# Kernel tuning notes

Measured on AMD Instinct MI355X. Metric: run time of the kernel, lower is better.

Reference implementation:

```python
import jax, jax.numpy as jnp
import numpy as np

WH, WW = 7, 7
NUM_HEADS = 16
DIM = 512
NW = 64  # windows per image (56/7)^2


def _relative_position_index(wh, ww):
    coords = np.stack(np.meshgrid(np.arange(wh), np.arange(ww), indexing='ij'))  # 2,wh,ww
    cf = coords.reshape(2, -1)
    rel = cf[:, :, None] - cf[:, None, :]            # 2,N,N
    rel = rel.transpose(1, 2, 0).astype(np.int32)    # N,N,2
    rel[:, :, 0] += wh - 1
    rel[:, :, 1] += ww - 1
    rel[:, :, 0] *= 2 * ww - 1
    return jnp.asarray(rel.sum(-1))                  # N,N int32


def setup_inputs() -> dict:
    key = jax.random.key(0)
    ks = jax.random.split(key, 7)
    B_, N, C = 2048, WH * WW, DIM
    x = jax.random.normal(ks[0], (B_, N, C), dtype=jnp.float32)
    # 0 / -100 shifted-window mask pattern
    mask = jnp.where(jax.random.uniform(ks[1], (NW, N, N)) < 0.8, 0.0, -100.0).astype(jnp.float32)
    qkv_w = jax.random.normal(ks[2], (3 * C, C), dtype=jnp.float32) * 0.02
    qkv_b = jax.random.normal(ks[3], (3 * C,), dtype=jnp.float32) * 0.02
    proj_w = jax.random.normal(ks[4], (C, C), dtype=jnp.float32) * 0.02
    proj_b = jax.random.normal(ks[5], (C,), dtype=jnp.float32) * 0.02
    rel_bias_table = jax.random.normal(ks[6], ((2 * WH - 1) * (2 * WW - 1), NUM_HEADS), dtype=jnp.float32) * 0.02
    rel_index = _relative_position_index(WH, WW)
    return {"x": x, "mask": mask, "qkv_w": qkv_w, "qkv_b": qkv_b,
            "proj_w": proj_w, "proj_b": proj_b,
            "rel_bias_table": rel_bias_table, "rel_index": rel_index}


def reference(x, mask, qkv_w, qkv_b, proj_w, proj_b, rel_bias_table, rel_index):
    B_, N, C = x.shape
    H = NUM_HEADS
    hd = C // H
    scale = hd ** -0.5
    qkv = x @ qkv_w.T + qkv_b                         # B_,N,3C
    qkv = qkv.reshape(B_, N, 3, H, hd).transpose(2, 0, 3, 1, 4)  # 3,B_,H,N,hd
    q, k, v = qkv[0] * scale, qkv[1], qkv[2]
    attn = jnp.einsum('bhnd,bhmd->bhnm', q, k)        # B_,H,N,N
    # gathered relative position bias -> H,N,N
    bias = rel_bias_table[rel_index.reshape(-1)].reshape(N, N, H).transpose(2, 0, 1)
    attn = attn + bias[None]
    nW = mask.shape[0]
    attn = attn.reshape(B_ // nW, nW, H, N, N) + mask[None, :, None]
    attn = jax.nn.softmax(attn.reshape(B_, H, N, N), axis=-1)
    out = jnp.einsum('bhnm,bhmd->bhnd', attn, v).transpose(0, 2, 1, 3).reshape(B_, N, C)
    return out @ proj_w.T + proj_b
```

## Files before the change

### kernel.cpp

```cpp
#include <hip/hip_runtime.h>

typedef unsigned short u16;
typedef short s16x8 __attribute__((ext_vector_type(8)));
typedef __bf16 bf16x8 __attribute__((ext_vector_type(8)));
typedef float f32x4 __attribute__((ext_vector_type(4)));


__device__ __forceinline__ u16 f2bf(float f) {
  union { float f; unsigned u; } x; x.f = f;
  unsigned r = (x.u + 0x7fffu + ((x.u >> 16) & 1u)) >> 16;
  return (u16)r;
}

__device__ __forceinline__ f32x4 mfma_bf16_16x16x32(s16x8 a, s16x8 b, f32x4 c) {
  return __builtin_amdgcn_mfma_f32_16x16x32_bf16(
      __builtin_bit_cast(bf16x8, a), __builtin_bit_cast(bf16x8, b), c, 0, 0, 0);
}

__device__ __forceinline__ void gl_lds16(const u16* g, u16* l) {
  __builtin_amdgcn_global_load_lds(
      (__attribute__((address_space(1))) unsigned int*)g,
      (__attribute__((address_space(3))) unsigned int*)l, 16, 0, 0);
}

__device__ __forceinline__ int p_idx(int row, int col) {
  return row * 64 + ((((col >> 3) ^ (row & 7)) << 3) | (col & 7));
}


__global__ __launch_bounds__(256) void cvt_bf16(const float* __restrict__ src,
                                                u16* __restrict__ dst, int n) {
  int i = (blockIdx.x * 256 + threadIdx.x) * 4;
  if (i + 3 < n) {
    float4 f = *(const float4*)(src + i);
    ushort4 o;
    o.x = f2bf(f.x); o.y = f2bf(f.y); o.z = f2bf(f.z); o.w = f2bf(f.w);
    *(ushort4*)(dst + i) = o;
  }
}

__global__ __launch_bounds__(256) void build_bias(const float* __restrict__ tbl,
                                                  const int* __restrict__ ridx,
                                                  float* __restrict__ biasf) {
  int t = blockIdx.x * 256 + threadIdx.x;
  if (t < 16 * 2401) {
    int h = t / 2401, ij = t % 2401;
    biasf[t] = tbl[ridx[ij] * 16 + h];
  }
}


template <bool OUT_BF16>
__global__ __launch_bounds__(256) void gemm_bt(const u16* __restrict__ A,
                                               const u16* __restrict__ B,
                                               const float* __restrict__ bias,
                                               void* __restrict__ C,
                                               int M, int N, int K) {
  __shared__ u16 As[2][128 * 32];
  __shared__ u16 Bs[2][128 * 32];
  const int t = threadIdx.x;
  const int w = t >> 6, l = t & 63;
  const int quad = l >> 4, lo = l & 15;

  int bx = blockIdx.x, by = blockIdx.y;
  {
    const int nwg = gridDim.x * gridDim.y;
    if ((nwg & 7) == 0) {
      const int lin = bx + gridDim.x * by;
      const int swz = (lin & 7) * (nwg >> 3) + (lin >> 3);
      bx = swz % gridDim.x;
      by = swz / gridDim.x;
    }
  }
  const long m0 = (long)by * 128;
  const long n0 = (long)bx * 128;
  const int wm = (w >> 1) * 64, wn = (w & 1) * 64;

  f32x4 acc[4][4] = {};

  const int srow0 = w * 32 + (l >> 2);
  const int skc = ((l & 3) ^ ((srow0 >> 1) & 3)) * 8;
  const u16* gA = A + (m0 + srow0) * (long)K + skc;
  const u16* gB = B + (n0 + srow0) * (long)K + skc;
  const int lofs = (w * 128 + l) * 8;

  const int NT = K >> 5;

  gl_lds16(gA, As[0] + lofs);
  gl_lds16(gA + 16 * (long)K, As[0] + lofs + 64 * 8);
  gl_lds16(gB, Bs[0] + lofs);
  gl_lds16(gB + 16 * (long)K, Bs[0] + lofs + 64 * 8);
  __syncthreads();

  int cur = 0;
  for (int t0 = 0; t0 < NT; ++t0) {
    if (t0 + 1 < NT) {
      const int k0 = (t0 + 1) << 5;
      gl_lds16(gA + k0, As[cur ^ 1] + lofs);
      gl_lds16(gA + 16 * (long)K + k0, As[cur ^ 1] + lofs + 64 * 8);
      gl_lds16(gB + k0, Bs[cur ^ 1] + lofs);
      gl_lds16(gB + 16 * (long)K + k0, Bs[cur ^ 1] + lofs + 64 * 8);
    }

    const u16* as = As[cur];
    const u16* bs = Bs[cur];
    s16x8 af[4], bfv[4];
#pragma unroll
    for (int i = 0; i < 4; ++i) {
      const int ra = wm + i * 16 + lo;
      const int rb = wn + i * 16 + lo;
      af[i]  = *(const s16x8*)(as + ra * 32 + ((quad ^ ((ra >> 1) & 3)) << 3));
      bfv[i] = *(const s16x8*)(bs + rb * 32 + ((quad ^ ((rb >> 1) & 3)) << 3));
    }
#pragma unroll
    for (int mt = 0; mt < 4; ++mt)
#pragma unroll
      for (int nt = 0; nt < 4; ++nt)
        acc[mt][nt] = mfma_bf16_16x16x32(af[mt], bfv[nt], acc[mt][nt]);

    __syncthreads();
    cur ^= 1;
  }

#pragma unroll
  for (int mt = 0; mt < 4; ++mt) {
#pragma unroll
    for (int nt = 0; nt < 4; ++nt) {
      long col = n0 + wn + nt * 16 + lo;
      float bv = bias[col];
      long rowb = m0 + wm + mt * 16 + quad * 4;
#pragma unroll
      for (int r = 0; r < 4; ++r) {
        float v = acc[mt][nt][r] + bv;
        long off = (rowb + r) * (long)N + col;
        if (OUT_BF16) ((u16*)C)[off] = f2bf(v);
        else          ((float*)C)[off] = v;
      }
    }
  }
}


__global__ __launch_bounds__(256) void attn_kernel(const u16* __restrict__ qkv,
                                                   const float* __restrict__ biasf,
                                                   const float* __restrict__ mask,
                                                   u16* __restrict__ ao) {
  __shared__ u16 P[4][64 * 64];
  const int t = threadIdx.x;
  const int w = t >> 6, l = t & 63;
  const int quad = l >> 4, lo = l & 15;
  const int u = blockIdx.x * 4 + w;
  const int b = u >> 4, h = u & 15;

  const u16* qp = qkv + (long)b * 49 * 1536 + h * 32;
  const u16* kp = qp + 512;
  const u16* vp = qp + 1024;

  const s16x8 zero8 = {};
  s16x8 qf[4], kf[4];
#pragma unroll
  for (int mt = 0; mt < 4; ++mt) {
    int m = mt * 16 + lo;
    qf[mt] = (m < 49) ? *(const s16x8*)(qp + (long)m * 1536 + quad * 8) : zero8;
    kf[mt] = (m < 49) ? *(const s16x8*)(kp + (long)m * 1536 + quad * 8) : zero8;
  }

  f32x4 S[4][4] = {};
#pragma unroll
  for (int mt = 0; mt < 4; ++mt)
#pragma unroll
    for (int nt = 0; nt < 4; ++nt)
      S[mt][nt] = mfma_bf16_16x16x32(qf[mt], kf[nt], S[mt][nt]);

  const float scale = 0.17677669529663687f;
  const float* bh = biasf + h * 2401;
  const float* mw = mask + (long)(b & 63) * 2401;

#pragma unroll
  for (int mt = 0; mt < 4; ++mt) {
#pragma unroll
    for (int r = 0; r < 4; ++r) {
      int row = mt * 16 + quad * 4 + r;
      int rr = row < 49 ? row : 48;
      float vals[4];
#pragma unroll
      for (int nt = 0; nt < 4; ++nt) {
        int col = nt * 16 + lo;
        vals[nt] = (col < 49)
                       ? S[mt][nt][r] * scale + bh[rr * 49 + col] + mw[rr * 49 + col]
                       : -1e30f;
      }
      float rm = fmaxf(fmaxf(vals[0], vals[1]), fmaxf(vals[2], vals[3]));
#pragma unroll
      for (int off = 1; off < 16; off <<= 1) rm = fmaxf(rm, __shfl_xor(rm, off, 16));
      float s = 0.f;
#pragma unroll
      for (int nt = 0; nt < 4; ++nt) {
        vals[nt] = __expf(vals[nt] - rm);
        s += vals[nt];
      }
#pragma unroll
      for (int off = 1; off < 16; off <<= 1) s += __shfl_xor(s, off, 16);
      float is = 1.f / s;
#pragma unroll
      for (int nt = 0; nt < 4; ++nt) S[mt][nt][r] = vals[nt] * is;
    }
  }

  u16* pw = &P[w][0];
#pragma unroll
  for (int mt = 0; mt < 4; ++mt)
#pragma unroll
    for (int nt = 0; nt < 4; ++nt)
#pragma unroll
      for (int r = 0; r < 4; ++r)
        pw[p_idx(mt * 16 + quad * 4 + r, nt * 16 + lo)] = f2bf(S[mt][nt][r]);

  f32x4 O[4][2] = {};
#pragma unroll
  for (int kt = 0; kt < 2; ++kt) {
    s16x8 vb[2];
#pragma unroll
    for (int nt = 0; nt < 2; ++nt) {
      union { u16 us[8]; s16x8 v; } tb;
#pragma unroll
      for (int jj = 0; jj < 8; ++jj) {
        int j = kt * 32 + quad * 8 + jj;
        tb.us[jj] = (j < 49) ? vp[(long)j * 1536 + nt * 16 + lo] : (u16)0;
      }
      vb[nt] = tb.v;
    }
#pragma unroll
    for (int mt = 0; mt < 4; ++mt) {
      s16x8 pa = *(const s16x8*)(pw + p_idx(mt * 16 + lo, kt * 32 + quad * 8));
      O[mt][0] = mfma_bf16_16x16x32(pa, vb[0], O[mt][0]);
      O[mt][1] = mfma_bf16_16x16x32(pa, vb[1], O[mt][1]);
    }
  }

  u16* op = ao + (long)b * 49 * 512 + h * 32;
#pragma unroll
  for (int mt = 0; mt < 4; ++mt)
#pragma unroll
    for (int nt = 0; nt < 2; ++nt)
#pragma unroll
      for (int r = 0; r < 4; ++r) {
        int row = mt * 16 + quad * 4 + r;
        if (row < 49) op[(long)row * 512 + nt * 16 + lo] = f2bf(O[mt][nt][r]);
      }
}


extern "C" void kernel_launch(void* const* d_in, const int* in_sizes, int n_in,
                              void* d_out, int out_size, void* d_ws, size_t ws_size,
                              hipStream_t stream) {
  const float* x      = (const float*)d_in[0];
  const float* mask   = (const float*)d_in[1];
  const float* qkv_w  = (const float*)d_in[2];
  const float* qkv_b  = (const float*)d_in[3];
  const float* proj_w = (const float*)d_in[4];
  const float* proj_b = (const float*)d_in[5];
  const float* tbl    = (const float*)d_in[6];
  const int*   ridx   = (const int*)d_in[7];

  u16* xb    = (u16*)d_ws;
  u16* qkvb  = xb + 51380224;
  u16* wq    = qkvb + 154140672;
  u16* wp    = wq + 786432;
  float* biasf = (float*)(wp + 262144);

  cvt_bf16<<<50176, 256, 0, stream>>>(x, xb, 51380224);
  cvt_bf16<<<768, 256, 0, stream>>>(qkv_w, wq, 786432);
  cvt_bf16<<<256, 256, 0, stream>>>(proj_w, wp, 262144);
  build_bias<<<151, 256, 0, stream>>>(tbl, ridx, biasf);

  gemm_bt<true><<<dim3(12, 784), 256, 0, stream>>>(xb, wq, qkv_b, qkvb,
                                                   100352, 1536, 512);
  attn_kernel<<<8192, 256, 0, stream>>>(qkvb, biasf, mask, xb);

  gemm_bt<false><<<dim3(4, 784), 256, 0, stream>>>(xb, wp, proj_b, d_out,
                                                   100352, 512, 512);
}
```

Baseline: 899.5 us.

## Triple-buffer GEMM LDS tiles with prefetch distance two and partial vmcnt waits

```diff
diff --git a/kernel.cpp b/kernel.cpp
--- a/kernel.cpp
+++ b/kernel.cpp
@@ -56,8 +56,8 @@
                                                const float* __restrict__ bias,
                                                void* __restrict__ C,
                                                int M, int N, int K) {
-  __shared__ u16 As[2][128 * 32];
-  __shared__ u16 Bs[2][128 * 32];
+  __shared__ u16 As[3][128 * 32];
+  __shared__ u16 Bs[3][128 * 32];
   const int t = threadIdx.x;
   const int w = t >> 6, l = t & 63;
   const int quad = l >> 4, lo = l & 15;
@@ -86,21 +86,25 @@
 
   const int NT = K >> 5;
 
-  gl_lds16(gA, As[0] + lofs);
-  gl_lds16(gA + 16 * (long)K, As[0] + lofs + 64 * 8);
-  gl_lds16(gB, Bs[0] + lofs);
-  gl_lds16(gB + 16 * (long)K, Bs[0] + lofs + 64 * 8);
-  __syncthreads();
+  auto STAGE = [&](int tile, int buf) {
+    const int k0 = tile << 5;
+    gl_lds16(gA + k0, As[buf] + lofs);
+    gl_lds16(gA + 16 * (long)K + k0, As[buf] + lofs + 64 * 8);
+    gl_lds16(gB + k0, Bs[buf] + lofs);
+    gl_lds16(gB + 16 * (long)K + k0, Bs[buf] + lofs + 64 * 8);
+  };
+
+  STAGE(0, 0);
+  STAGE(1, 1);
+  asm volatile("s_waitcnt vmcnt(4)" ::: "memory");
+  __builtin_amdgcn_sched_barrier(0);
+  __builtin_amdgcn_s_barrier();
+  __builtin_amdgcn_sched_barrier(0);
 
   int cur = 0;
   for (int t0 = 0; t0 < NT; ++t0) {
-    if (t0 + 1 < NT) {
-      const int k0 = (t0 + 1) << 5;
-      gl_lds16(gA + k0, As[cur ^ 1] + lofs);
-      gl_lds16(gA + 16 * (long)K + k0, As[cur ^ 1] + lofs + 64 * 8);
-      gl_lds16(gB + k0, Bs[cur ^ 1] + lofs);
-      gl_lds16(gB + 16 * (long)K + k0, Bs[cur ^ 1] + lofs + 64 * 8);
-    }
+    int wb = cur + 2; if (wb >= 3) wb -= 3;
+    if (t0 + 2 < NT) STAGE(t0 + 2, wb);
 
     const u16* as = As[cur];
     const u16* bs = Bs[cur];
@@ -118,8 +122,15 @@
       for (int nt = 0; nt < 4; ++nt)
         acc[mt][nt] = mfma_bf16_16x16x32(af[mt], bfv[nt], acc[mt][nt]);
 
-    __syncthreads();
-    cur ^= 1;
+    if (t0 + 2 < NT) {
+      asm volatile("s_waitcnt vmcnt(4)" ::: "memory");
+    } else {
+      asm volatile("s_waitcnt vmcnt(0)" ::: "memory");
+    }
+    __builtin_amdgcn_sched_barrier(0);
+    __builtin_amdgcn_s_barrier();
+    __builtin_amdgcn_sched_barrier(0);
+    ++cur; if (cur == 3) cur = 0;
   }
 
 #pragma unroll
```

Result: no change. 903.1 us (+0.4%).
